# Kernel tuning notes

Measured on AMD Instinct MI355X. Metric: run time of the kernel, lower is better.

Reference implementation:

```python
import jax, jax.numpy as jnp
import numpy as np

B = 256
LSTM = 512
FEAT = 3 * 3 * 512 + 16 + 8  # 4632
N_ACT = 4
ACT_SHAPE = 64
NUM_STEPS = 20
CANVAS_IN = 6 * 32 * 32  # 6144
H1 = int(FEAT / (FEAT / LSTM) ** (1.0 / 3.0))  # 2223
H2 = int(FEAT / (FEAT / LSTM) ** (2.0 / 3.0))  # 1067


def setup_inputs() -> dict:
    key = jax.random.key(0)
    ks = jax.random.split(key, 32)

    def g(k, shape, scale=0.02):
        return jax.random.normal(k, shape, dtype=jnp.float32) * scale

    inp = {
        "actualCanvas": jax.random.normal(ks[0], (B, 3, 32, 32), dtype=jnp.float32),
        "objectiveCanvas": jax.random.normal(ks[1], (B, 3, 32, 32), dtype=jnp.float32),
        "last_action_end_position": jax.random.randint(ks[2], (B,), 0, ACT_SHAPE),
        "episode_percentage": jax.random.randint(ks[3], (B,), 0, NUM_STEPS),
        # feature extractor stub (flatten -> linear -> relu), output 4608
        "Wfe": g(ks[4], (4608, CANVAS_IN)), "bfe": jnp.zeros((4608,), jnp.float32),
        "emb_end": g(ks[5], (ACT_SHAPE, 16), 1.0),
        "emb_ep": g(ks[6], (NUM_STEPS, 8), 1.0),
        "W1": g(ks[7], (H1, FEAT)), "b1": jnp.zeros((H1,), jnp.float32),
        "W2": g(ks[8], (H2, H1)), "b2": jnp.zeros((H2,), jnp.float32),
        "W3": g(ks[9], (LSTM, H2)), "b3": jnp.zeros((LSTM,), jnp.float32),
        "W_ih": g(ks[10], (4 * LSTM, LSTM)), "W_hh": g(ks[11], (4 * LSTM, LSTM)),
        "b_ih": jnp.zeros((4 * LSTM,), jnp.float32), "b_hh": jnp.zeros((4 * LSTM,), jnp.float32),
        "Wd1": g(ks[12], (N_ACT, LSTM // 2, LSTM)), "bd1": jnp.zeros((N_ACT, LSTM // 2), jnp.float32),
        "Wd2": g(ks[13], (N_ACT, ACT_SHAPE, LSTM // 2)), "bd2": jnp.zeros((N_ACT, ACT_SHAPE), jnp.float32),
        "emb_dec": g(ks[14], (N_ACT, ACT_SHAPE, 16), 1.0),
        "Wout": g(ks[15], (LSTM, LSTM + 16)), "bout": jnp.zeros((LSTM,), jnp.float32),
    }
    return inp


def reference(actualCanvas, objectiveCanvas, last_action_end_position, episode_percentage,
              Wfe, bfe, emb_end, emb_ep, W1, b1, W2, b2, W3, b3,
              W_ih, W_hh, b_ih, b_hh, Wd1, bd1, Wd2, bd2, emb_dec, Wout, bout):
    # feature extractor on channel-concatenated canvases -> [B, 4608]
    x = jnp.concatenate([actualCanvas, objectiveCanvas], axis=1).reshape(B, -1)
    fv = jax.nn.relu(x @ Wfe.T + bfe)
    feats = jnp.concatenate([fv, emb_end[last_action_end_position], emb_ep[episode_percentage]], axis=1)
    # fc1->fc2->fc3 (dropout = eval mode / identity)
    h = jax.nn.relu(feats @ W1.T + b1)
    h = jax.nn.relu(h @ W2.T + b2)
    h = jax.nn.relu(h @ W3.T + b3)  # [B, LSTM]
    # single-step LSTM with zero initial state (first execution)
    gates = h @ W_ih.T + b_ih + b_hh  # h0 = 0 so recurrent matmul vanishes
    i, f, g_, o = jnp.split(gates, 4, axis=1)
    c = jax.nn.sigmoid(i) * jnp.tanh(g_)
    seed = jax.nn.sigmoid(o) * jnp.tanh(c)  # [B, LSTM]
    z = seed
    log_probabilities = jnp.zeros((B,), jnp.float32)
    entropy = jnp.float32(0.0)
    actions = []
    base_key = jax.random.key(42)
    for k in range(N_ACT):
        hm = jax.nn.relu(z @ Wd1[k].T + bd1[k])
        logits = hm @ Wd2[k].T + bd2[k]  # [B, ACT_SHAPE]
        logp = jax.nn.log_softmax(logits, axis=1)
        probs = jnp.exp(logp)
        entropy = entropy + jnp.sum(-probs * logp)
        act = jax.random.categorical(jax.random.fold_in(base_key, k), logits, axis=1)  # [B]
        actions.append(act)
        log_probabilities = log_probabilities + jnp.take_along_axis(logp, act[:, None], axis=1)[:, 0]
        emb_a = emb_dec[k][act]  # [B,16]
        z = jax.nn.relu(jnp.concatenate([z, emb_a], axis=1) @ Wout.T + bout)
    action = jnp.stack(actions, axis=1)  # [B, N_ACT]
    return action, entropy, log_probabilities
```

## Files before the change

kernel.cpp:

```cpp
#include <hip/hip_runtime.h>
#include <hip/hip_bf16.h>
#include <stdint.h>

#define B_SZ   256
#define LSTM_N 512
#define FEAT_N 4632
#define FV_N   4608
#define CIN_N  6144
#define HALF_CIN 3072
#define ACT_N  64
#define LD_FEAT 4672
#define LD_ZEXT 576

typedef __attribute__((ext_vector_type(8))) short bf16x8;
typedef __attribute__((ext_vector_type(4))) float f32x4;

__device__ __forceinline__ short f2bf(float f) {
  uint32_t u = __float_as_uint(f);
  u += 0x7FFFu + ((u >> 16) & 1u);
  return (short)(u >> 16);
}
__device__ __forceinline__ float bf2f(short s) {
  return __uint_as_float(((uint32_t)(uint16_t)s) << 16);
}
__device__ __forceinline__ uint32_t pack2(float x, float y) {
  return (__float_as_uint(x) >> 16) | (__float_as_uint(y) & 0xffff0000u);
}

typedef __attribute__((address_space(3))) void lds_void_t;
typedef const __attribute__((address_space(1))) void gbl_void_t;
__device__ __forceinline__ void lds_dma16(const void* g, void* l) {
  __builtin_amdgcn_global_load_lds((gbl_void_t*)g, (lds_void_t*)l, 16, 0, 0);
}

__device__ __forceinline__ uint32_t rotl32(uint32_t x, int r) {
  return (x << r) | (x >> (32 - r));
}
__device__ __forceinline__ void threefry2x32(uint32_t k0, uint32_t k1,
                                             uint32_t x0, uint32_t x1,
                                             uint32_t& o0, uint32_t& o1) {
  uint32_t k2 = k0 ^ k1 ^ 0x1BD11BDAu;
  x0 += k0; x1 += k1;
  x0 += x1; x1 = rotl32(x1, 13); x1 ^= x0;
  x0 += x1; x1 = rotl32(x1, 15); x1 ^= x0;
  x0 += x1; x1 = rotl32(x1, 26); x1 ^= x0;
  x0 += x1; x1 = rotl32(x1,  6); x1 ^= x0;
  x0 += k1; x1 += k2 + 1u;
  x0 += x1; x1 = rotl32(x1, 17); x1 ^= x0;
  x0 += x1; x1 = rotl32(x1, 29); x1 ^= x0;
  x0 += x1; x1 = rotl32(x1, 16); x1 ^= x0;
  x0 += x1; x1 = rotl32(x1, 24); x1 ^= x0;
  x0 += k2; x1 += k0 + 2u;
  x0 += x1; x1 = rotl32(x1, 13); x1 ^= x0;
  x0 += x1; x1 = rotl32(x1, 15); x1 ^= x0;
  x0 += x1; x1 = rotl32(x1, 26); x1 ^= x0;
  x0 += x1; x1 = rotl32(x1,  6); x1 ^= x0;
  x0 += k0; x1 += k1 + 3u;
  x0 += x1; x1 = rotl32(x1, 17); x1 ^= x0;
  x0 += x1; x1 = rotl32(x1, 29); x1 ^= x0;
  x0 += x1; x1 = rotl32(x1, 16); x1 ^= x0;
  x0 += x1; x1 = rotl32(x1, 24); x1 ^= x0;
  x0 += k1; x1 += k2 + 4u;
  x0 += x1; x1 = rotl32(x1, 13); x1 ^= x0;
  x0 += x1; x1 = rotl32(x1, 15); x1 ^= x0;
  x0 += x1; x1 = rotl32(x1, 26); x1 ^= x0;
  x0 += x1; x1 = rotl32(x1,  6); x1 ^= x0;
  x0 += k2; x1 += k0 + 5u;
  o0 = x0; o1 = x1;
}

__global__ void concat_cvt_kernel(const float* __restrict__ act,
                                  const float* __restrict__ obj,
                                  short* __restrict__ xb) {
  int idx = blockIdx.x * 256 + threadIdx.x;
  if (idx >= B_SZ * 768) return;
  int row = idx / 768;
  int c8 = (idx - row * 768) * 8;
  const float* src = (c8 < HALF_CIN) ? (act + (size_t)row * HALF_CIN + c8)
                                     : (obj + (size_t)row * HALF_CIN + (c8 - HALF_CIN));
  float4 u = ((const float4*)src)[0];
  float4 v = ((const float4*)src)[1];
  bf16x8 r;
  r[0]=f2bf(u.x); r[1]=f2bf(u.y); r[2]=f2bf(u.z); r[3]=f2bf(u.w);
  r[4]=f2bf(v.x); r[5]=f2bf(v.y); r[6]=f2bf(v.z); r[7]=f2bf(v.w);
  *(bf16x8*)&xb[(size_t)row * CIN_N + c8] = r;
}

__global__ void gumbel_kernel(float* __restrict__ gum) {
  int idx = blockIdx.x * 256 + threadIdx.x;
  if (idx >= 4 * 16384) return;
  int k = idx >> 14;
  uint32_t j = (uint32_t)(idx & 16383);
  uint32_t f0, f1, o0, o1, bits;
  threefry2x32(0u, 42u, 0u, (uint32_t)k, f0, f1);
  if (j < 8192u) { threefry2x32(f0, f1, j, j + 8192u, o0, o1); bits = o0; }
  else           { threefry2x32(f0, f1, j - 8192u, j, o0, o1); bits = o1; }
  const float tiny = 1.17549435e-38f;
  float fu = __uint_as_float((bits >> 9) | 0x3f800000u) - 1.0f;
  float u = fmaxf(tiny, fu * (1.0f - tiny) + tiny);
  gum[idx] = -logf(-logf(u));
}

__global__ void fill_embs_kernel(const int* __restrict__ lastpos,
                                 const int* __restrict__ ep,
                                 const float* __restrict__ emb_end,
                                 const float* __restrict__ emb_ep,
                                 short* __restrict__ feats) {
  int b = blockIdx.x;
  int t = threadIdx.x;
  short* row = feats + (size_t)b * LD_FEAT;
  if (t < 16)      row[FV_N + t] = f2bf(emb_end[lastpos[b] * 16 + t]);
  else if (t < 24) row[FV_N + 16 + (t - 16)] = f2bf(emb_ep[ep[b] * 8 + (t - 16)]);
  else             row[FV_N + t] = 0;
}

__global__ __launch_bounds__(512, 6) void gemm6_kernel(
    const short* __restrict__ A, int ldab,
    const float* __restrict__ W, int ldw,
    const float* __restrict__ Wend,
    short* __restrict__ P, int nblk,
    int N, int Kiter, int kc, int nchunks) {
  __shared__ float Wlds[2][64 * 64];

  const int tid = threadIdx.x;
  const int w = tid >> 6, l = tid & 63, l15 = l & 15, lg = l >> 4;
  const int mb = blockIdx.x & 1;
  const int n0 = (blockIdx.x >> 1) * 64;
  const int Np = nblk * 64;
  const int ks = blockIdx.y;
  const int kbeg = ks * kc;
  const int kend = (kbeg + kc < Kiter) ? (kbeg + kc) : Kiter;
  const int nk = (kend - kbeg) >> 6;
  const int mrow = mb * 128 + (w << 4);

  const char* wlim = (const char*)Wend - 16;

  f32x4 acc[4];
#pragma unroll
  for (int j = 0; j < 4; ++j) acc[j] = (f32x4){0.f, 0.f, 0.f, 0.f};

  auto dma = [&](int kt, int buf) {
#pragma unroll
    for (int q = 0; q < 2; ++q) {
      int r = (w << 3) + (q << 2) + (l >> 4);
      int gn = n0 + r; if (gn >= N) gn = N - 1;
      int g16 = (l & 15) ^ (r & 15);
      const char* src = (const char*)(W + (size_t)gn * ldw + kt) + g16 * 16;
      if (src > wlim) src = wlim;
      lds_dma16(src, (void*)&Wlds[buf][((w << 3) + (q << 2)) * 64]);
    }
  };

  if (nk > 0) {
    dma(kbeg, 0);
    __syncthreads();

    for (int t = 0; t < nk; ++t) {
      const int cur = t & 1;
      const int kt = kbeg + (t << 6);
      if (t + 1 < nk) dma(kt + 64, cur ^ 1);
      const short* arow = &A[(size_t)(mrow + l15) * ldab + kt + (lg << 3)];
      bf16x8 af0 = *(const bf16x8*)arow;
      bf16x8 af1 = *(const bf16x8*)(arow + 32);
#pragma unroll
      for (int nj = 0; nj < 4; ++nj) {
        int r = (nj << 4) + l15;
        const float* rb = &Wlds[cur][r * 64];
        int rx = r & 15;
        f32x4 u0 = *(const f32x4*)(rb + ((((lg << 1)    ) ^ rx) << 2));
        f32x4 u1 = *(const f32x4*)(rb + ((((lg << 1) | 1) ^ rx) << 2));
        f32x4 v0 = *(const f32x4*)(rb + ((((lg << 1) + 8) ^ rx) << 2));
        f32x4 v1 = *(const f32x4*)(rb + ((((lg << 1) + 9) ^ rx) << 2));
        bf16x8 b0, b1;
        uint32_t* p0 = (uint32_t*)&b0;
        uint32_t* p1 = (uint32_t*)&b1;
        p0[0] = pack2(u0[0], u0[1]); p0[1] = pack2(u0[2], u0[3]);
        p0[2] = pack2(u1[0], u1[1]); p0[3] = pack2(u1[2], u1[3]);
        p1[0] = pack2(v0[0], v0[1]); p1[1] = pack2(v0[2], v0[3]);
        p1[2] = pack2(v1[0], v1[1]); p1[3] = pack2(v1[2], v1[3]);
        acc[nj] = __builtin_amdgcn_mfma_f32_16x16x32_bf16(af0, b0, acc[nj], 0, 0, 0);
        acc[nj] = __builtin_amdgcn_mfma_f32_16x16x32_bf16(af1, b1, acc[nj], 0, 0, 0);
      }
      __syncthreads();
    }
  }

  short* Pb = P + (size_t)ks * 256 * Np;
#pragma unroll
  for (int nj = 0; nj < 4; ++nj) {
    int gn = n0 + (nj << 4) + l15;
#pragma unroll
    for (int r = 0; r < 4; ++r) {
      int gm = mrow + (lg << 2) + r;
      Pb[(size_t)gm * Np + gn] = f2bf(acc[nj][r]);
    }
  }
}

__global__ void reduce_kernel(const short* __restrict__ P, int Np, int nchunks,
                              const float* __restrict__ bias1,
                              const float* __restrict__ bias2,
                              void* __restrict__ out, int ldc, int N,
                              int relu, int mode_f32) {
  int npack = Np >> 3;
  int idx = blockIdx.x * 256 + threadIdx.x;
  if (idx >= 256 * npack) return;
  int m = idx / npack;
  int n8 = (idx - m * npack) << 3;
  float s[8] = {0.f, 0.f, 0.f, 0.f, 0.f, 0.f, 0.f, 0.f};
  for (int ks = 0; ks < nchunks; ++ks) {
    bf16x8 v = *(const bf16x8*)&P[(size_t)ks * 256 * Np + (size_t)m * Np + n8];
#pragma unroll
    for (int j = 0; j < 8; ++j) s[j] += bf2f(v[j]);
  }
#pragma unroll
  for (int j = 0; j < 8; ++j) {
    int n = n8 + j;
    float r = 0.f;
    if (n < N) {
      r = s[j];
      if (bias1) r += bias1[n];
      if (bias2) r += bias2[n];
      if (relu) r = fmaxf(r, 0.f);
    }
    s[j] = r;
  }
  if (mode_f32) {
    float* o = (float*)out + (size_t)m * ldc + n8;
#pragma unroll
    for (int j = 0; j < 8; ++j) o[j] = s[j];
  } else {
    bf16x8 r;
#pragma unroll
    for (int j = 0; j < 8; ++j) r[j] = f2bf(s[j]);
    *(bf16x8*)((short*)out + (size_t)m * ldc + n8) = r;
  }
}

__global__ void reduce_lstm_kernel(const short* __restrict__ P, int nchunks,
                                   const float* __restrict__ b_ih,
                                   const float* __restrict__ b_hh,
                                   short* __restrict__ zext) {
  int idx = blockIdx.x * 256 + threadIdx.x;
  if (idx >= 256 * 64) return;
  int m = idx >> 6;
  int n8 = (idx & 63) << 3;
  float gi[8] = {}, gg[8] = {}, go[8] = {};
  for (int ks = 0; ks < nchunks; ++ks) {
    const short* base = P + ((size_t)ks * 256 + m) * 2048;
    bf16x8 vi = *(const bf16x8*)(base + n8);
    bf16x8 vg = *(const bf16x8*)(base + 1024 + n8);
    bf16x8 vo = *(const bf16x8*)(base + 1536 + n8);
#pragma unroll
    for (int j = 0; j < 8; ++j) {
      gi[j] += bf2f(vi[j]); gg[j] += bf2f(vg[j]); go[j] += bf2f(vo[j]);
    }
  }
  bf16x8 hv;
#pragma unroll
  for (int j = 0; j < 8; ++j) {
    int n = n8 + j;
    float i_ = gi[j] + b_ih[n] + b_hh[n];
    float g_ = gg[j] + b_ih[1024 + n] + b_hh[1024 + n];
    float o_ = go[j] + b_ih[1536 + n] + b_hh[1536 + n];
    float si = 1.f / (1.f + expf(-i_));
    float so = 1.f / (1.f + expf(-o_));
    float c = si * tanhf(g_);
    hv[j] = f2bf(so * tanhf(c));
  }
  *(bf16x8*)&zext[(size_t)m * LD_ZEXT + n8] = hv;
}

__global__ __launch_bounds__(256) void logits_sample_kernel(
    const short* __restrict__ hm,
    const float* __restrict__ Wd2k,
    const float* __restrict__ bd2k,
    const float* __restrict__ gumk,
    const float* __restrict__ embk,
    short* __restrict__ zext,
    int* __restrict__ act_out, float* __restrict__ logp_out,
    float* __restrict__ ent_out, int write_emb) {
  __shared__ short Wl[64 * 264];
  const int tid = threadIdx.x;
  const int w = tid >> 6, l = tid & 63, l15 = l & 15, lg = l >> 4;
  const int mbase = blockIdx.x * 64 + w * 16;

  {
    int r = tid >> 2;
    int c0 = (tid & 3) << 6;
    const float* src = Wd2k + r * 256 + c0;
    short* dst = &Wl[r * 264 + c0];
#pragma unroll
    for (int i = 0; i < 8; ++i) {
      float4 u = ((const float4*)src)[2 * i];
      float4 v = ((const float4*)src)[2 * i + 1];
      bf16x8 t;
      t[0]=f2bf(u.x); t[1]=f2bf(u.y); t[2]=f2bf(u.z); t[3]=f2bf(u.w);
      t[4]=f2bf(v.x); t[5]=f2bf(v.y); t[6]=f2bf(v.z); t[7]=f2bf(v.w);
      *(bf16x8*)(dst + 8 * i) = t;
    }
  }
  __syncthreads();

  f32x4 acc[4];
#pragma unroll
  for (int j = 0; j < 4; ++j) acc[j] = (f32x4){0.f, 0.f, 0.f, 0.f};

#pragma unroll
  for (int kt = 0; kt < 4; ++kt) {
    int k0 = kt << 6;
    const short* arow = &hm[(size_t)(mbase + l15) * 256 + k0 + (lg << 3)];
    bf16x8 af0 = *(const bf16x8*)arow;
    bf16x8 af1 = *(const bf16x8*)(arow + 32);
#pragma unroll
    for (int nj = 0; nj < 4; ++nj) {
      const short* bp = &Wl[((nj << 4) + l15) * 264 + k0 + (lg << 3)];
      bf16x8 b0 = *(const bf16x8*)bp;
      bf16x8 b1 = *(const bf16x8*)(bp + 32);
      acc[nj] = __builtin_amdgcn_mfma_f32_16x16x32_bf16(af0, b0, acc[nj], 0, 0, 0);
      acc[nj] = __builtin_amdgcn_mfma_f32_16x16x32_bf16(af1, b1, acc[nj], 0, 0, 0);
    }
  }

  float bcol[4];
#pragma unroll
  for (int nj = 0; nj < 4; ++nj) bcol[nj] = bd2k[(nj << 4) + l15];

#pragma unroll
  for (int r = 0; r < 4; ++r) {
    int row = mbase + (lg << 2) + r;
    float lv[4];
#pragma unroll
    for (int nj = 0; nj < 4; ++nj) lv[nj] = acc[nj][r] + bcol[nj];
    float mx = fmaxf(fmaxf(lv[0], lv[1]), fmaxf(lv[2], lv[3]));
#pragma unroll
    for (int off = 8; off; off >>= 1) mx = fmaxf(mx, __shfl_xor(mx, off));
    float es = expf(lv[0]-mx) + expf(lv[1]-mx) + expf(lv[2]-mx) + expf(lv[3]-mx);
#pragma unroll
    for (int off = 8; off; off >>= 1) es += __shfl_xor(es, off);
    float lse = logf(es);
    float lp[4], ent = 0.f;
#pragma unroll
    for (int nj = 0; nj < 4; ++nj) {
      lp[nj] = lv[nj] - mx - lse;
      ent += -expf(lp[nj]) * lp[nj];
    }
#pragma unroll
    for (int off = 8; off; off >>= 1) ent += __shfl_xor(ent, off);
    float bv = -3.4e38f; int bc = 64; float blp = 0.f;
#pragma unroll
    for (int nj = 0; nj < 4; ++nj) {
      int col = (nj << 4) + l15;
      float pert = lv[nj] + gumk[row * 64 + col];
      if (pert > bv || (pert == bv && col < bc)) { bv = pert; bc = col; blp = lp[nj]; }
    }
#pragma unroll
    for (int off = 8; off; off >>= 1) {
      float ov = __shfl_xor(bv, off);
      int oc = __shfl_xor(bc, off);
      float olp = __shfl_xor(blp, off);
      if (ov > bv || (ov == bv && oc < bc)) { bv = ov; bc = oc; blp = olp; }
    }
    if (l15 == 0) {
      act_out[row] = bc;
      logp_out[row] = blp;
      ent_out[row] = ent;
    }
    if (write_emb) {
      short* zr = zext + (size_t)row * LD_ZEXT;
      zr[512 + l15] = f2bf(embk[bc * 16 + l15]);
      zr[528 + l15] = 0;
      zr[544 + l15] = 0;
      zr[560 + l15] = 0;
    }
  }
}

__global__ void finalize_kernel(const int* __restrict__ act,
                                const float* __restrict__ logp_k,
                                const float* __restrict__ ent,
                                float* __restrict__ out) {
  __shared__ float sred[4];
  int t = threadIdx.x;
#pragma unroll
  for (int k = 0; k < 4; ++k)
    out[t * 4 + k] = (float)act[k * 256 + t];
  float lp = 0.f;
#pragma unroll
  for (int k = 0; k < 4; ++k) lp += logp_k[k * 256 + t];
  out[1025 + t] = lp;

  float v = 0.f;
#pragma unroll
  for (int k = 0; k < 4; ++k) v += ent[k * 256 + t];
#pragma unroll
  for (int off = 32; off; off >>= 1) v += __shfl_xor(v, off);
  if ((t & 63) == 0) sred[t >> 6] = v;
  __syncthreads();
  if (t == 0) out[1024] = sred[0] + sred[1] + sred[2] + sred[3];
}

extern "C" void kernel_launch(void* const* d_in, const int* in_sizes, int n_in,
                              void* d_out, int out_size, void* d_ws, size_t ws_size,
                              hipStream_t stream) {
  float* out = (float*)d_out;
  char* out_bytes = (char*)d_out;
  auto sentinel = [&](int code) { hipMemsetAsync(out_bytes + 4096, code, 4, stream); };

  if (n_in < 25 || in_sizes[0] != B_SZ * 3 * 32 * 32 ||
      in_sizes[4] != FV_N * CIN_N || in_sizes[23] != LSTM_N * 528 ||
      in_sizes[9] <= 0 || in_sizes[9] > 8192 ||
      in_sizes[11] <= 0 || in_sizes[11] > 8192) {
    sentinel(0x42);
    return;
  }

  const float* actual = (const float*)d_in[0];
  const float* object = (const float*)d_in[1];
  const int* lastpos  = (const int*)d_in[2];
  const int* ep       = (const int*)d_in[3];
  const float* Wfe    = (const float*)d_in[4];
  const float* bfe    = (const float*)d_in[5];
  const float* emb_end= (const float*)d_in[6];
  const float* emb_ep = (const float*)d_in[7];
  const float* W1     = (const float*)d_in[8];
  const float* b1     = (const float*)d_in[9];
  const float* W2     = (const float*)d_in[10];
  const float* b2     = (const float*)d_in[11];
  const float* W3     = (const float*)d_in[12];
  const float* b3     = (const float*)d_in[13];
  const float* W_ih   = (const float*)d_in[14];
  const float* b_ih   = (const float*)d_in[16];
  const float* b_hh   = (const float*)d_in[17];
  const float* Wd1    = (const float*)d_in[18];
  const float* bd1    = (const float*)d_in[19];
  const float* Wd2    = (const float*)d_in[20];
  const float* bd2    = (const float*)d_in[21];
  const float* embdec = (const float*)d_in[22];
  const float* Wout   = (const float*)d_in[23];
  const float* bout   = (const float*)d_in[24];

  const int H1 = in_sizes[9];
  const int H2 = in_sizes[11];
  const int ldh1 = 64 * ((H1 + 63) / 64);
  const int ldh2 = 64 * ((H2 + 63) / 64);

  char* wsb = (char*)d_ws;
  size_t off = 0;
  auto alloc = [&](size_t bytes) {
    char* p = wsb + off;
    off += (bytes + 255) & ~(size_t)255;
    return p;
  };
  float* logpk = (float*)alloc(1024 * 4);
  float* entk  = (float*)alloc(1024 * 4);
  int*   actk  = (int*)alloc(1024 * 4);
  float* gumb  = (float*)alloc(4 * 16384 * 4);
  short* xb    = (short*)alloc((size_t)B_SZ * CIN_N * 2);
  short* feats = (short*)alloc((size_t)B_SZ * LD_FEAT * 2);
  short* h1    = (short*)alloc((size_t)B_SZ * ldh1 * 2);
  short* h2    = (short*)alloc((size_t)B_SZ * ldh2 * 2);
  short* h3    = (short*)alloc((size_t)B_SZ * 512 * 2);
  short* zextA = (short*)alloc((size_t)B_SZ * LD_ZEXT * 2);
  short* zextB = (short*)alloc((size_t)B_SZ * LD_ZEXT * 2);
  short* hm    = (short*)alloc((size_t)B_SZ * 256 * 2);
  if (off + (8 << 20) > ws_size) {
    sentinel(0x43);
    return;
  }
  short* slab = (short*)(wsb + off);
  const size_t slab_bytes = ws_size - off;

  auto gemm = [&](const short* A, int ldab, const float* Wm, int ldw, int Kiter,
                  const float* bb1, const float* bb2,
                  void* C, int ldc, int N, int relu, int fuse) {
    int nblk = (N + 63) / 64;
    int Np = nblk * 64;
    int tiles = Kiter >> 6;
    int c = (384 + nblk - 1) / nblk;
    if (c > tiles) c = tiles;
    size_t cap = slab_bytes / ((size_t)256 * Np * 2);
    if ((size_t)c > cap) c = (int)cap;
    if (c < 1) c = 1;
    int ct = (tiles + c - 1) / c;
    int kc = 64 * ct;
    int chunks = (tiles + ct - 1) / ct;
    dim3 g(2 * nblk, chunks);
    gemm6_kernel<<<g, dim3(512), 0, stream>>>(
        A, ldab, Wm, ldw, Wm + (size_t)N * ldw, slab, nblk, N, Kiter, kc, chunks);
    if (fuse == 1) {
      reduce_lstm_kernel<<<dim3(64), dim3(256), 0, stream>>>(
          slab, chunks, bb1, bb2, (short*)C);
    } else {
      int npack = Np >> 3;
      reduce_kernel<<<dim3((256 * npack + 255) / 256), dim3(256), 0, stream>>>(
          slab, Np, chunks, bb1, bb2, C, ldc, N, relu, 0);
    }
  };

  concat_cvt_kernel<<<dim3(768), dim3(256), 0, stream>>>(actual, object, xb);
  gumbel_kernel<<<dim3(256), dim3(256), 0, stream>>>(gumb);
  gemm(xb, CIN_N, Wfe, CIN_N, CIN_N, bfe, nullptr, feats, LD_FEAT, FV_N, 1, 0);
  fill_embs_kernel<<<dim3(B_SZ), dim3(64), 0, stream>>>(lastpos, ep, emb_end, emb_ep, feats);
  gemm(feats, LD_FEAT, W1, FEAT_N, LD_FEAT, b1, nullptr, h1, ldh1, H1, 1, 0);
  gemm(h1, ldh1, W2, H1, ldh1, b2, nullptr, h2, ldh2, H2, 1, 0);
  gemm(h2, ldh2, W3, H2, ldh2, b3, nullptr, h3, 512, LSTM_N, 1, 0);
  gemm(h3, 512, W_ih, LSTM_N, 512, b_ih, b_hh, zextA, LD_ZEXT, 4 * LSTM_N, 0, 1);

  short* zcur = zextA;
  short* znxt = zextB;
  for (int k = 0; k < 4; ++k) {
    const float* Wd1k = Wd1 + (size_t)k * 256 * LSTM_N;
    const float* bd1k = bd1 + (size_t)k * 256;
    const float* Wd2k = Wd2 + (size_t)k * ACT_N * 256;
    const float* bd2k = bd2 + (size_t)k * ACT_N;
    const float* embk = embdec + (size_t)k * ACT_N * 16;
    gemm(zcur, LD_ZEXT, Wd1k, LSTM_N, 512, bd1k, nullptr, hm, 256, 256, 1, 0);
    logits_sample_kernel<<<dim3(4), dim3(256), 0, stream>>>(
        hm, Wd2k, bd2k, gumb + k * 16384, embk, zcur,
        actk + k * B_SZ, logpk + k * B_SZ, entk + k * B_SZ, (k < 3) ? 1 : 0);
    if (k < 3) {
      gemm(zcur, LD_ZEXT, Wout, 528, LD_ZEXT, bout, nullptr, znxt, LD_ZEXT, LSTM_N, 1, 0);
      short* t = zcur; zcur = znxt; znxt = t;
    }
  }

  finalize_kernel<<<dim3(1), dim3(256), 0, stream>>>(actk, logpk, entk, out);
}
```

Before: 263.9 us.

## Cover all 256 rows per GEMM block to reuse converted weight tiles

Each GEMM block now covers all 256 batch rows, with each wave computing two 16-row fragments, instead of splitting M into two 128-row halves. Every fp32-to-bf16 weight conversion from LDS now feeds twice as many MFMAs, and each weight tile is read from global memory once instead of twice. The split-K target rises from 384 to 512 blocks to make up for the halved grid width. In exchange it uses more accumulator registers (launch bounds lowered to 4), and the partial-sum slab and reduction grow.

```diff
diff --git a/kernel.cpp b/kernel.cpp
--- a/kernel.cpp
+++ b/kernel.cpp
@@ -114,7 +114,7 @@
   else             row[FV_N + t] = 0;
 }
 
-__global__ __launch_bounds__(512, 6) void gemm6_kernel(
+__global__ __launch_bounds__(512, 4) void gemm7_kernel(
     const short* __restrict__ A, int ldab,
     const float* __restrict__ W, int ldw,
     const float* __restrict__ Wend,
@@ -124,20 +124,21 @@
 
   const int tid = threadIdx.x;
   const int w = tid >> 6, l = tid & 63, l15 = l & 15, lg = l >> 4;
-  const int mb = blockIdx.x & 1;
-  const int n0 = (blockIdx.x >> 1) * 64;
+  const int n0 = blockIdx.x * 64;
   const int Np = nblk * 64;
   const int ks = blockIdx.y;
   const int kbeg = ks * kc;
   const int kend = (kbeg + kc < Kiter) ? (kbeg + kc) : Kiter;
   const int nk = (kend - kbeg) >> 6;
-  const int mrow = mb * 128 + (w << 4);
+  const int mrow = w << 5;
 
   const char* wlim = (const char*)Wend - 16;
 
-  f32x4 acc[4];
-#pragma unroll
-  for (int j = 0; j < 4; ++j) acc[j] = (f32x4){0.f, 0.f, 0.f, 0.f};
+  f32x4 acc[2][4];
+#pragma unroll
+  for (int i = 0; i < 2; ++i)
+#pragma unroll
+    for (int j = 0; j < 4; ++j) acc[i][j] = (f32x4){0.f, 0.f, 0.f, 0.f};
 
   auto dma = [&](int kt, int buf) {
 #pragma unroll
@@ -158,10 +159,14 @@
     for (int t = 0; t < nk; ++t) {
       const int cur = t & 1;
       const int kt = kbeg + (t << 6);
+      bf16x8 af[2][2];
+#pragma unroll
+      for (int mf = 0; mf < 2; ++mf) {
+        const short* arow = &A[(size_t)(mrow + (mf << 4) + l15) * ldab + kt + (lg << 3)];
+        af[mf][0] = *(const bf16x8*)arow;
+        af[mf][1] = *(const bf16x8*)(arow + 32);
+      }
       if (t + 1 < nk) dma(kt + 64, cur ^ 1);
-      const short* arow = &A[(size_t)(mrow + l15) * ldab + kt + (lg << 3)];
-      bf16x8 af0 = *(const bf16x8*)arow;
-      bf16x8 af1 = *(const bf16x8*)(arow + 32);
 #pragma unroll
       for (int nj = 0; nj < 4; ++nj) {
         int r = (nj << 4) + l15;
@@ -178,8 +183,10 @@
         p0[2] = pack2(u1[0], u1[1]); p0[3] = pack2(u1[2], u1[3]);
         p1[0] = pack2(v0[0], v0[1]); p1[1] = pack2(v0[2], v0[3]);
         p1[2] = pack2(v1[0], v1[1]); p1[3] = pack2(v1[2], v1[3]);
-        acc[nj] = __builtin_amdgcn_mfma_f32_16x16x32_bf16(af0, b0, acc[nj], 0, 0, 0);
-        acc[nj] = __builtin_amdgcn_mfma_f32_16x16x32_bf16(af1, b1, acc[nj], 0, 0, 0);
+        acc[0][nj] = __builtin_amdgcn_mfma_f32_16x16x32_bf16(af[0][0], b0, acc[0][nj], 0, 0, 0);
+        acc[1][nj] = __builtin_amdgcn_mfma_f32_16x16x32_bf16(af[1][0], b0, acc[1][nj], 0, 0, 0);
+        acc[0][nj] = __builtin_amdgcn_mfma_f32_16x16x32_bf16(af[0][1], b1, acc[0][nj], 0, 0, 0);
+        acc[1][nj] = __builtin_amdgcn_mfma_f32_16x16x32_bf16(af[1][1], b1, acc[1][nj], 0, 0, 0);
       }
       __syncthreads();
     }
@@ -190,10 +197,12 @@
   for (int nj = 0; nj < 4; ++nj) {
     int gn = n0 + (nj << 4) + l15;
 #pragma unroll
-    for (int r = 0; r < 4; ++r) {
-      int gm = mrow + (lg << 2) + r;
-      Pb[(size_t)gm * Np + gn] = f2bf(acc[nj][r]);
-    }
+    for (int mf = 0; mf < 2; ++mf)
+#pragma unroll
+      for (int r = 0; r < 4; ++r) {
+        int gm = mrow + (mf << 4) + (lg << 2) + r;
+        Pb[(size_t)gm * Np + gn] = f2bf(acc[mf][nj][r]);
+      }
   }
 }
 
@@ -477,7 +486,7 @@
     int nblk = (N + 63) / 64;
     int Np = nblk * 64;
     int tiles = Kiter >> 6;
-    int c = (384 + nblk - 1) / nblk;
+    int c = (512 + nblk - 1) / nblk;
     if (c > tiles) c = tiles;
     size_t cap = slab_bytes / ((size_t)256 * Np * 2);
     if ((size_t)c > cap) c = (int)cap;
@@ -485,8 +494,8 @@
     int ct = (tiles + c - 1) / c;
     int kc = 64 * ct;
     int chunks = (tiles + ct - 1) / ct;
-    dim3 g(2 * nblk, chunks);
-    gemm6_kernel<<<g, dim3(512), 0, stream>>>(
+    dim3 g(nblk, chunks);
+    gemm7_kernel<<<g, dim3(512), 0, stream>>>(
         A, ldab, Wm, ldw, Wm + (size_t)N * ldw, slab, nblk, N, Kiter, kc, chunks);
     if (fuse == 1) {
       reduce_lstm_kernel<<<dim3(64), dim3(256), 0, stream>>>(
```

Measured after the change: 274.1 us. +3.9%, slower.
